# Optimization experiments

Measured on AMD Instinct MI355X. Metric: run time of the kernel, lower is better.

The kernel has to match this reference:

```python
import jax, jax.numpy as jnp
import numpy as np

L_MAX = 5
C_IN = 24
HIDDEN = 32
BATCH = 256


def _valid_pairs(l):
    return [(l1, l2) for l1 in range(L_MAX + 1) for l2 in range(L_MAX + 1)
            if abs(l1 - l2) <= l <= l1 + l2]


def _make_cg():
    # Packed padded CG coefficient tensor cg[l1, l2, l, m, m1, m2].
    # Values are fixed deterministic constants; sparsity follows the true
    # selection rule m = m1 + m2 (indices stored shifted by +l).
    D = 2 * L_MAX + 1
    rng = np.random.RandomState(42)
    cg = np.zeros((L_MAX + 1, L_MAX + 1, L_MAX + 1, D, D, D), dtype=np.float32)
    for l in range(L_MAX + 1):
        for (l1, l2) in _valid_pairs(l):
            m = np.arange(-l, l + 1)[:, None, None]
            m1 = np.arange(-l1, l1 + 1)[None, :, None]
            m2 = np.arange(-l2, l2 + 1)[None, None, :]
            mask = (m == m1 + m2).astype(np.float32)
            vals = rng.randn(2 * l + 1, 2 * l1 + 1, 2 * l2 + 1).astype(np.float32)
            cg[l1, l2, l, :2 * l + 1, :2 * l1 + 1, :2 * l2 + 1] = vals * mask
    return jnp.asarray(cg)


def setup_inputs() -> dict:
    key = jax.random.key(0)
    keys = jax.random.split(key, 12)
    inp = {}
    for l in range(L_MAX + 1):
        inp[f"x{l}"] = jax.random.normal(keys[l], (BATCH, C_IN, 2 * l + 1), dtype=jnp.float32)
    for l in range(L_MAX + 1):
        k_in = len(_valid_pairs(l)) * C_IN * C_IN
        scale = 1.0 / np.sqrt(k_in)
        inp[f"W{l}"] = jax.random.normal(keys[6 + l], (HIDDEN, k_in), dtype=jnp.float32) * scale
    inp["cg"] = _make_cg()
    return inp


def reference(x0, x1, x2, x3, x4, x5, W0, W1, W2, W3, W4, W5, cg):
    xs = [x0, x1, x2, x3, x4, x5]
    Ws = [W0, W1, W2, W3, W4, W5]
    outs = []
    for l in range(L_MAX + 1):
        feats = []
        for (l1, l2) in _valid_pairs(l):
            c = cg[l1, l2, l, :2 * l + 1, :2 * l1 + 1, :2 * l2 + 1]  # [2l+1, 2l1+1, 2l2+1]
            # P[b, c1, c2, m] = sum_{m1,m2} cg[m,m1,m2] x_l1[b,c1,m1] x_l2[b,c2,m2]
            p = jnp.einsum('mij,bci,bdj->bcdm', c, xs[l1], xs[l2])
            feats.append(p.reshape(p.shape[0], -1, 2 * l + 1))
        cat = jnp.concatenate(feats, axis=1)  # [B, n_pairs*C*C, 2l+1]
        outs.append(jnp.einsum('hk,bkm->bhm', Ws[l], cat))  # [B, HIDDEN, 2l+1]
    # concat orders along the m axis -> [B, HIDDEN, sum_l (2l+1) = 36]
    return jnp.concatenate(outs, axis=-1)
```

## Files before the change

### kernel.cpp

```cpp
#include <hip/hip_runtime.h>
#include <hip/hip_bf16.h>

typedef __attribute__((ext_vector_type(8))) short bf16x8;
typedef __attribute__((ext_vector_type(4))) float f32x4;
typedef __attribute__((ext_vector_type(2))) float f32x2;

struct Params {
  const float* x[6];
  const float* W[6];
  const float* cg;
  float* out;
  unsigned short* Wb;
};

constexpr int NPAIRS_C[6] = {6, 15, 21, 24, 24, 21};
constexpr int POFF_C[6]   = {0, 6, 21, 42, 66, 90};
constexpr size_t WBASE_C[6] = {0, 110592, 387072, 774144, 1216512, 1658880};
constexpr int KL_C[6]   = {3456, 8640, 12096, 13824, 13824, 12096};
constexpr int LOFF_C[6] = {0, 1, 4, 9, 16, 25};
#define XSTRIDE 204

constexpr int TL1[111] = {
  0,1,2,3,4,5,
  0,1,1,1,2,2,2,3,3,3,4,4,4,5,5,
  0,1,1,1,2,2,2,2,2,3,3,3,3,3,4,4,4,4,5,5,5,
  0,1,1,1,2,2,2,2,2,3,3,3,3,3,3,4,4,4,4,4,5,5,5,5,
  0,1,1,1,2,2,2,2,3,3,3,3,3,4,4,4,4,4,4,5,5,5,5,5,
  0,1,1,2,2,2,3,3,3,3,4,4,4,4,4,5,5,5,5,5,5
};
constexpr int TL2R[111] = {
  0,1,2,3,4,5,
  1,0,1,2,1,2,3,2,3,4,3,4,5,4,5,
  2,1,2,3,0,1,2,3,4,1,2,3,4,5,2,3,4,5,3,4,5,
  3,2,3,4,1,2,3,4,5,0,1,2,3,4,5,1,2,3,4,5,2,3,4,5,
  4,3,4,5,2,3,4,5,1,2,3,4,5,0,1,2,3,4,5,1,2,3,4,5,
  5,4,5,3,4,5,2,3,4,5,1,2,3,4,5,0,1,2,3,4,5
};

__constant__ int c_l1[111] = {
  0,1,2,3,4,5,
  0,1,1,1,2,2,2,3,3,3,4,4,4,5,5,
  0,1,1,1,2,2,2,2,2,3,3,3,3,3,4,4,4,4,5,5,5,
  0,1,1,1,2,2,2,2,2,3,3,3,3,3,3,4,4,4,4,4,5,5,5,5,
  0,1,1,1,2,2,2,2,3,3,3,3,3,4,4,4,4,4,4,5,5,5,5,5,
  0,1,1,2,2,2,3,3,3,3,4,4,4,4,4,5,5,5,5,5,5
};
__constant__ int c_l2[111] = {
  0,1,2,3,4,5,
  1,0,1,2,1,2,3,2,3,4,3,4,5,4,5,
  2,1,2,3,0,1,2,3,4,1,2,3,4,5,2,3,4,5,3,4,5,
  3,2,3,4,1,2,3,4,5,0,1,2,3,4,5,1,2,3,4,5,2,3,4,5,
  4,3,4,5,2,3,4,5,1,2,3,4,5,0,1,2,3,4,5,1,2,3,4,5,
  5,4,5,3,4,5,2,3,4,5,1,2,3,4,5,0,1,2,3,4,5
};
__constant__ int c_mb_l[21]  = {5,5,5,5,5,5, 4,4,4,4,4, 3,3,3,3, 2,2,2, 1,1, 0};
__constant__ int c_mb_m0[21] = {0,2,4,6,8,10, 0,2,4,6,8, 0,2,4,6, 0,2,4, 0,2, 0};
__constant__ int c_GA3[6] = {0,1,2,9,10,11};

template<int L>
__device__ __forceinline__ void swz(const Params& P, int u8) {
  constexpr int KL = KL_C[L];
  constexpr int KL8 = KL / 8;
  if (u8 >= 32 * KL8) return;
  const int h  = u8 / KL8;
  const int k  = (u8 - h * KL8) * 8;
  const int pair = k / 576;
  const int kin  = k - pair * 576;
  const int kc = kin >> 5;
  const int g  = (kin >> 3) & 3;
  const float* src = P.W[L] + (size_t)h * KL + k;
  f32x4 v0 = *(const f32x4*)src;
  f32x4 v1 = *(const f32x4*)(src + 4);
  union { __hip_bfloat162 h2; unsigned int u; } z;
  unsigned int o0, o1, o2, o3;
  z.h2 = __float22bfloat162_rn(make_float2(v0.x, v0.y)); o0 = z.u;
  z.h2 = __float22bfloat162_rn(make_float2(v0.z, v0.w)); o1 = z.u;
  z.h2 = __float22bfloat162_rn(make_float2(v1.x, v1.y)); o2 = z.u;
  z.h2 = __float22bfloat162_rn(make_float2(v1.z, v1.w)); o3 = z.u;
  const size_t dst = WBASE_C[L] + (size_t)pair * 18432 + kc * 1024 + (h >> 4) * 512
                   + ((size_t)(g * 16 + (h & 15))) * 8;
  *(uint4*)(P.Wb + dst) = make_uint4(o0, o1, o2, o3);
}

__global__ __launch_bounds__(256)
void swizzle_W(Params P) {
  const int u8 = blockIdx.x * 256 + threadIdx.x;
  switch (blockIdx.y) {
    case 0: swz<0>(P, u8); break;
    case 1: swz<1>(P, u8); break;
    case 2: swz<2>(P, u8); break;
    case 3: swz<3>(P, u8); break;
    case 4: swz<4>(P, u8); break;
    default: swz<5>(P, u8); break;
  }
}

#define XALL_F 0
#define CG_F   7344
#define RED_F  7920
#define SMEM_FLOATS 10992

template<int L>
__device__ __forceinline__ void body(const Params& P, const int mp0, const int btile) {
  constexpr int NP  = NPAIRS_C[L];
  constexpr int OFF = POFF_C[L];
  extern __shared__ float smem[];
  float* xall  = smem + XALL_F;
  float* cgall = smem + CG_F;
  float* red   = smem + RED_F;

  const int t    = threadIdx.x;
  const int lane = t & 63;
  const int w    = t >> 6;
  const int q8   = lane >> 4;
  const int rI   = lane & 15;
  const int b    = rI & 7;
  const int mpL  = rI >> 3;
  const int b0   = btile * 8;

#pragma unroll
  for (int l = 0; l < 6; ++l) {
    const int n = 2 * l + 1;
    const float* src = P.x[l] + (size_t)b0 * 24 * n;
    const int tot = 8 * 24 * n;
    for (int e = t; e < tot; e += 384) {
      const int bc = e / n;
      const int i  = e - bc * n;
      xall[(LOFF_C[l] + i) * XSTRIDE + bc] = src[e];
    }
  }
  for (int e = t; e < 2 * NP * 12; e += 384) {
    const int i  = e % 12;
    const int r  = e / 12;
    const int pi = r % NP;
    const int mL = r / NP;
    const int l1 = c_l1[OFF + pi], l2 = c_l2[OFF + pi];
    const int mp = mp0 + mL;
    const int j  = mp + l1 + l2 - L - i;
    float v = 0.f;
    if (mp <= 2 * L && i <= 2 * l1 && j >= 0 && j <= 2 * l2)
      v = P.cg[((size_t)(((l1 * 6 + l2) * 6 + L) * 11 + mp) * 11 + i) * 11 + j];
    cgall[(mL * NP + pi) * 12 + i] = v;
  }
  __syncthreads();

  f32x4 accC0 = {0.f, 0.f, 0.f, 0.f};
  f32x4 accC1 = {0.f, 0.f, 0.f, 0.f};
  const int colb = b * 24;

  const int kcA = c_GA3[w];
  const int k0  = kcA * 32 + q8 * 8;
  const int cA  = k0 / 24;
  const int d0  = k0 - cA * 24;
  const float* x2base = xall + colb + d0;
  const float* x1base = xall + colb + cA;

#pragma unroll
  for (int pi = 0; pi < NP; ++pi) {
    const int l1 = TL1[OFF + pi], l2 = TL2R[OFF + pi];
    const int n1 = 2 * l1 + 1, n2 = 2 * l2 + 1;
    const int R1 = LOFF_C[l1], R2 = LOFF_C[l2];
    const int mK0w = mp0 + l1 + l2 - L;
    const int mK0l = mK0w + mpL;
    const int i0 = (mK0w - (n2 - 1)) > 0 ? (mK0w - (n2 - 1)) : 0;
    const int i1 = (n1 - 1) < (mK0w + 1) ? (n1 - 1) : (mK0w + 1);

    const unsigned short* wbp = P.Wb + WBASE_C[L] + (size_t)pi * 18432 + lane * 8;
    const bf16x8 wfA0 = *(const bf16x8*)(wbp + kcA * 1024);
    const bf16x8 wfA1 = *(const bf16x8*)(wbp + kcA * 1024 + 512);
    const bf16x8 wfB0 = *(const bf16x8*)(wbp + (kcA + 3) * 1024);
    const bf16x8 wfB1 = *(const bf16x8*)(wbp + (kcA + 3) * 1024 + 512);
    const bf16x8 wfC0 = *(const bf16x8*)(wbp + (kcA + 6) * 1024);
    const bf16x8 wfC1 = *(const bf16x8*)(wbp + (kcA + 6) * 1024 + 512);

    f32x2 pA[4], pB[4], pC[4];
#pragma unroll
    for (int dd = 0; dd < 4; ++dd) {
      pA[dd] = (f32x2){0.f, 0.f};
      pB[dd] = (f32x2){0.f, 0.f};
      pC[dd] = (f32x2){0.f, 0.f};
    }

    const float* cgp = cgall + (mpL * NP + pi) * 12;
    for (int i = i0; i <= i1; ++i) {
      const float cgv = cgp[i];
      int j = mK0l - i;
      j = j < 0 ? 0 : (j > n2 - 1 ? n2 - 1 : j);
      const float* x2p = x2base + (R2 + j) * XSTRIDE;
      f32x2 xv[4];
      *(f32x4*)&xv[0] = *(const f32x4*)x2p;
      *(f32x4*)&xv[2] = *(const f32x4*)(x2p + 4);
      const float* x1p = x1base + (R1 + i) * XSTRIDE;
      const float sA = cgv * x1p[0];
      const float sB = cgv * x1p[4];
      const float sC = cgv * x1p[8];
      const f32x2 svA = {sA, sA}, svB = {sB, sB}, svC = {sC, sC};
#pragma unroll
      for (int dd = 0; dd < 4; ++dd) {
        pA[dd] += svA * xv[dd];
        pB[dd] += svB * xv[dd];
        pC[dd] += svC * xv[dd];
      }
    }
    union { unsigned int u[4]; bf16x8 v; } zA, zB, zC;
#pragma unroll
    for (int dd = 0; dd < 4; ++dd) {
      union { __hip_bfloat162 h2; unsigned int u; } z;
      z.h2 = __float22bfloat162_rn(make_float2(pA[dd].x, pA[dd].y)); zA.u[dd] = z.u;
      z.h2 = __float22bfloat162_rn(make_float2(pB[dd].x, pB[dd].y)); zB.u[dd] = z.u;
      z.h2 = __float22bfloat162_rn(make_float2(pC[dd].x, pC[dd].y)); zC.u[dd] = z.u;
    }
    accC0 = __builtin_amdgcn_mfma_f32_16x16x32_bf16(zA.v, wfA0, accC0, 0, 0, 0);
    accC0 = __builtin_amdgcn_mfma_f32_16x16x32_bf16(zB.v, wfB0, accC0, 0, 0, 0);
    accC0 = __builtin_amdgcn_mfma_f32_16x16x32_bf16(zC.v, wfC0, accC0, 0, 0, 0);
    accC1 = __builtin_amdgcn_mfma_f32_16x16x32_bf16(zA.v, wfA1, accC1, 0, 0, 0);
    accC1 = __builtin_amdgcn_mfma_f32_16x16x32_bf16(zB.v, wfB1, accC1, 0, 0, 0);
    accC1 = __builtin_amdgcn_mfma_f32_16x16x32_bf16(zC.v, wfC1, accC1, 0, 0, 0);
  }

  {
    const int col16 = lane & 15;
    const int rbase = w * 16 + (lane >> 4) * 4;
#pragma unroll
    for (int r = 0; r < 4; ++r) {
      red[(rbase + r) * 32 + col16]      = accC0[r];
      red[(rbase + r) * 32 + 16 + col16] = accC1[r];
    }
  }
  __syncthreads();
  for (int idx = t; idx < 512; idx += 384) {
    const int row = idx >> 5, h = idx & 31;
    float v = 0.f;
#pragma unroll
    for (int ww = 0; ww < 6; ++ww) v += red[ww * 512 + row * 32 + h];
    const int ob = row & 7, omL = row >> 3;
    const int mp = mp0 + omL;
    if (mp <= 2 * L)
      P.out[(size_t)(b0 + ob) * 1152 + h * 36 + L * L + mp] = v;
  }
}

__global__ __launch_bounds__(384, 5)
void CGLayer_main(Params P) {
  const int mb = blockIdx.x;
  const int l = c_mb_l[mb], mp0 = c_mb_m0[mb];
  const int btile = blockIdx.y;
  switch (l) {
    case 0: body<0>(P, mp0, btile); break;
    case 1: body<1>(P, mp0, btile); break;
    case 2: body<2>(P, mp0, btile); break;
    case 3: body<3>(P, mp0, btile); break;
    case 4: body<4>(P, mp0, btile); break;
    default: body<5>(P, mp0, btile); break;
  }
}

extern "C" void kernel_launch(void* const* d_in, const int* in_sizes, int n_in,
                              void* d_out, int out_size, void* d_ws, size_t ws_size,
                              hipStream_t stream) {
  Params P;
  for (int i = 0; i < 6; ++i) P.x[i] = (const float*)d_in[i];
  for (int i = 0; i < 6; ++i) P.W[i] = (const float*)d_in[6 + i];
  P.cg  = (const float*)d_in[12];
  P.out = (float*)d_out;
  P.Wb  = (unsigned short*)d_ws;

  dim3 sg(216, 6);
  swizzle_W<<<sg, 256, 0, stream>>>(P);
  dim3 grid(21, 32);
  CGLayer_main<<<grid, 384, SMEM_FLOATS * sizeof(float), stream>>>(P);
}
```

Baseline: 149.0 us.

## Specialize body on m-block offset, fully unroll CG inner loop, pad x smem layout

Turns the m-block start into a template parameter so the i-loop bounds per pair become compile-time constants, and fully unrolls the inner contraction loop. The j-index clamp is removed by adding zero guard rows and a per-lane row offset in shared memory. X storage moves to a padded per-batch stride (28) and a larger row stride, likely to cut LDS bank conflicts. This costs much more code (21 instantiations with full unrolling), which risks instruction-cache pressure, and it raises shared memory per block.

```diff
diff --git a/kernel.cpp b/kernel.cpp
--- a/kernel.cpp
+++ b/kernel.cpp
@@ -18,7 +18,8 @@
 constexpr size_t WBASE_C[6] = {0, 110592, 387072, 774144, 1216512, 1658880};
 constexpr int KL_C[6]   = {3456, 8640, 12096, 13824, 13824, 12096};
 constexpr int LOFF_C[6] = {0, 1, 4, 9, 16, 25};
-#define XSTRIDE 204
+#define XSTRIDE 236
+#define BSTRIDE 28
 
 constexpr int TL1[111] = {
   0,1,2,3,4,5,
@@ -53,8 +54,6 @@
   4,3,4,5,2,3,4,5,1,2,3,4,5,0,1,2,3,4,5,1,2,3,4,5,
   5,4,5,3,4,5,2,3,4,5,1,2,3,4,5,0,1,2,3,4,5
 };
-__constant__ int c_mb_l[21]  = {5,5,5,5,5,5, 4,4,4,4,4, 3,3,3,3, 2,2,2, 1,1, 0};
-__constant__ int c_mb_m0[21] = {0,2,4,6,8,10, 0,2,4,6,8, 0,2,4,6, 0,2,4, 0,2, 0};
 __constant__ int c_GA3[6] = {0,1,2,9,10,11};
 
 template<int L>
@@ -96,12 +95,12 @@
 }
 
 #define XALL_F 0
-#define CG_F   7344
-#define RED_F  7920
-#define SMEM_FLOATS 10992
-
-template<int L>
-__device__ __forceinline__ void body(const Params& P, const int mp0, const int btile) {
+#define CG_F   8968
+#define RED_F  9544
+#define SMEM_FLOATS 12616
+
+template<int L, int MP0>
+__device__ __forceinline__ void body(const Params& P, const int btile) {
   constexpr int NP  = NPAIRS_C[L];
   constexpr int OFF = POFF_C[L];
   extern __shared__ float smem[];
@@ -126,7 +125,9 @@
     for (int e = t; e < tot; e += 384) {
       const int bc = e / n;
       const int i  = e - bc * n;
-      xall[(LOFF_C[l] + i) * XSTRIDE + bc] = src[e];
+      const int bb = bc / 24;
+      const int cc = bc - 24 * bb;
+      xall[(1 + LOFF_C[l] + i) * XSTRIDE + bb * BSTRIDE + cc] = src[e];
     }
   }
   for (int e = t; e < 2 * NP * 12; e += 384) {
@@ -135,7 +136,7 @@
     const int pi = r % NP;
     const int mL = r / NP;
     const int l1 = c_l1[OFF + pi], l2 = c_l2[OFF + pi];
-    const int mp = mp0 + mL;
+    const int mp = MP0 + mL;
     const int j  = mp + l1 + l2 - L - i;
     float v = 0.f;
     if (mp <= 2 * L && i <= 2 * l1 && j >= 0 && j <= 2 * l2)
@@ -146,22 +147,21 @@
 
   f32x4 accC0 = {0.f, 0.f, 0.f, 0.f};
   f32x4 accC1 = {0.f, 0.f, 0.f, 0.f};
-  const int colb = b * 24;
 
   const int kcA = c_GA3[w];
   const int k0  = kcA * 32 + q8 * 8;
   const int cA  = k0 / 24;
   const int d0  = k0 - cA * 24;
-  const float* x2base = xall + colb + d0;
-  const float* x1base = xall + colb + cA;
+  const int bcol = b * BSTRIDE;
+  const float* x2l = xall + (size_t)(1 + mpL) * XSTRIDE + bcol + d0;
+  const float* x1l = xall + (size_t)1 * XSTRIDE + bcol + cA;
 
 #pragma unroll
   for (int pi = 0; pi < NP; ++pi) {
     const int l1 = TL1[OFF + pi], l2 = TL2R[OFF + pi];
     const int n1 = 2 * l1 + 1, n2 = 2 * l2 + 1;
     const int R1 = LOFF_C[l1], R2 = LOFF_C[l2];
-    const int mK0w = mp0 + l1 + l2 - L;
-    const int mK0l = mK0w + mpL;
+    const int mK0w = MP0 + l1 + l2 - L;
     const int i0 = (mK0w - (n2 - 1)) > 0 ? (mK0w - (n2 - 1)) : 0;
     const int i1 = (n1 - 1) < (mK0w + 1) ? (n1 - 1) : (mK0w + 1);
 
@@ -181,16 +181,17 @@
       pC[dd] = (f32x2){0.f, 0.f};
     }
 
-    const float* cgp = cgall + (mpL * NP + pi) * 12;
+    const float* cgp  = cgall + (mpL * NP + pi) * 12;
+    const float* x2pp = x2l + (size_t)(R2 + mK0w) * XSTRIDE;
+    const float* x1pp = x1l + (size_t)R1 * XSTRIDE;
+#pragma unroll
     for (int i = i0; i <= i1; ++i) {
       const float cgv = cgp[i];
-      int j = mK0l - i;
-      j = j < 0 ? 0 : (j > n2 - 1 ? n2 - 1 : j);
-      const float* x2p = x2base + (R2 + j) * XSTRIDE;
+      const float* x2p = x2pp - i * XSTRIDE;
       f32x2 xv[4];
       *(f32x4*)&xv[0] = *(const f32x4*)x2p;
       *(f32x4*)&xv[2] = *(const f32x4*)(x2p + 4);
-      const float* x1p = x1base + (R1 + i) * XSTRIDE;
+      const float* x1p = x1pp + i * XSTRIDE;
       const float sA = cgv * x1p[0];
       const float sB = cgv * x1p[4];
       const float sC = cgv * x1p[8];
@@ -234,7 +235,7 @@
 #pragma unroll
     for (int ww = 0; ww < 6; ++ww) v += red[ww * 512 + row * 32 + h];
     const int ob = row & 7, omL = row >> 3;
-    const int mp = mp0 + omL;
+    const int mp = MP0 + omL;
     if (mp <= 2 * L)
       P.out[(size_t)(b0 + ob) * 1152 + h * 36 + L * L + mp] = v;
   }
@@ -242,16 +243,29 @@
 
 __global__ __launch_bounds__(384, 5)
 void CGLayer_main(Params P) {
-  const int mb = blockIdx.x;
-  const int l = c_mb_l[mb], mp0 = c_mb_m0[mb];
-  const int btile = blockIdx.y;
-  switch (l) {
-    case 0: body<0>(P, mp0, btile); break;
-    case 1: body<1>(P, mp0, btile); break;
-    case 2: body<2>(P, mp0, btile); break;
-    case 3: body<3>(P, mp0, btile); break;
-    case 4: body<4>(P, mp0, btile); break;
-    default: body<5>(P, mp0, btile); break;
+  const int bt = blockIdx.y;
+  switch (blockIdx.x) {
+    case 0:  body<5, 0>(P, bt); break;
+    case 1:  body<5, 2>(P, bt); break;
+    case 2:  body<5, 4>(P, bt); break;
+    case 3:  body<5, 6>(P, bt); break;
+    case 4:  body<5, 8>(P, bt); break;
+    case 5:  body<5,10>(P, bt); break;
+    case 6:  body<4, 0>(P, bt); break;
+    case 7:  body<4, 2>(P, bt); break;
+    case 8:  body<4, 4>(P, bt); break;
+    case 9:  body<4, 6>(P, bt); break;
+    case 10: body<4, 8>(P, bt); break;
+    case 11: body<3, 0>(P, bt); break;
+    case 12: body<3, 2>(P, bt); break;
+    case 13: body<3, 4>(P, bt); break;
+    case 14: body<3, 6>(P, bt); break;
+    case 15: body<2, 0>(P, bt); break;
+    case 16: body<2, 2>(P, bt); break;
+    case 17: body<2, 4>(P, bt); break;
+    case 18: body<1, 0>(P, bt); break;
+    case 19: body<1, 2>(P, bt); break;
+    default: body<0, 0>(P, bt); break;
   }
 }
 
```

New measurement: 436.3 us. 193% more time.

## Split pair loop across two blocks with atomic output accumulation

Applied to the files above, without the earlier changes.

Doubles the grid by splitting each block's pair range into two halves, with each half accumulating into a zeroed output via atomicAdd (a memset is added before launch). The x tile in shared memory gets padding rows and a per-batch stride so the inner loop can drop the j clamp and use pointer increments. The reduction buffer now aliases the x buffer, which cuts shared-memory use and may raise occupancy. In exchange it adds an extra memset, atomics, a loop no longer fully unrolled with constant-memory lookups, and duplicated x loading per half.

```diff
diff --git a/kernel.cpp b/kernel.cpp
--- a/kernel.cpp
+++ b/kernel.cpp
@@ -17,25 +17,8 @@
 constexpr int POFF_C[6]   = {0, 6, 21, 42, 66, 90};
 constexpr size_t WBASE_C[6] = {0, 110592, 387072, 774144, 1216512, 1658880};
 constexpr int KL_C[6]   = {3456, 8640, 12096, 13824, 13824, 12096};
-constexpr int LOFF_C[6] = {0, 1, 4, 9, 16, 25};
-#define XSTRIDE 204
-
-constexpr int TL1[111] = {
-  0,1,2,3,4,5,
-  0,1,1,1,2,2,2,3,3,3,4,4,4,5,5,
-  0,1,1,1,2,2,2,2,2,3,3,3,3,3,4,4,4,4,5,5,5,
-  0,1,1,1,2,2,2,2,2,3,3,3,3,3,3,4,4,4,4,4,5,5,5,5,
-  0,1,1,1,2,2,2,2,3,3,3,3,3,4,4,4,4,4,4,5,5,5,5,5,
-  0,1,1,2,2,2,3,3,3,3,4,4,4,4,4,5,5,5,5,5,5
-};
-constexpr int TL2R[111] = {
-  0,1,2,3,4,5,
-  1,0,1,2,1,2,3,2,3,4,3,4,5,4,5,
-  2,1,2,3,0,1,2,3,4,1,2,3,4,5,2,3,4,5,3,4,5,
-  3,2,3,4,1,2,3,4,5,0,1,2,3,4,5,1,2,3,4,5,2,3,4,5,
-  4,3,4,5,2,3,4,5,1,2,3,4,5,0,1,2,3,4,5,1,2,3,4,5,
-  5,4,5,3,4,5,2,3,4,5,1,2,3,4,5,0,1,2,3,4,5
-};
+#define XSTRIDE 236
+#define BSTRIDE 28
 
 __constant__ int c_l1[111] = {
   0,1,2,3,4,5,
@@ -53,6 +36,7 @@
   4,3,4,5,2,3,4,5,1,2,3,4,5,0,1,2,3,4,5,1,2,3,4,5,
   5,4,5,3,4,5,2,3,4,5,1,2,3,4,5,0,1,2,3,4,5
 };
+__constant__ int c_loff[6] = {0, 1, 4, 9, 16, 25};
 __constant__ int c_mb_l[21]  = {5,5,5,5,5,5, 4,4,4,4,4, 3,3,3,3, 2,2,2, 1,1, 0};
 __constant__ int c_mb_m0[21] = {0,2,4,6,8,10, 0,2,4,6,8, 0,2,4,6, 0,2,4, 0,2, 0};
 __constant__ int c_GA3[6] = {0,1,2,9,10,11};
@@ -96,18 +80,18 @@
 }
 
 #define XALL_F 0
-#define CG_F   7344
-#define RED_F  7920
-#define SMEM_FLOATS 10992
+#define CG_F   8968
+#define SMEM_FLOATS 9544
 
 template<int L>
-__device__ __forceinline__ void body(const Params& P, const int mp0, const int btile) {
+__device__ __forceinline__ void body(const Params& P, const int mp0, const int btile,
+                                     const int half) {
   constexpr int NP  = NPAIRS_C[L];
   constexpr int OFF = POFF_C[L];
   extern __shared__ float smem[];
   float* xall  = smem + XALL_F;
   float* cgall = smem + CG_F;
-  float* red   = smem + RED_F;
+  float* red   = smem + XALL_F;
 
   const int t    = threadIdx.x;
   const int lane = t & 63;
@@ -117,7 +101,13 @@
   const int b    = rI & 7;
   const int mpL  = rI >> 3;
   const int b0   = btile * 8;
-
+  const int p0   = half ? NP / 2 : 0;
+  const int p1   = half ? NP : NP / 2;
+
+  for (int e = t; e < 2 * XSTRIDE; e += 384) {
+    const int r = (e < XSTRIDE) ? 0 : 37;
+    xall[r * XSTRIDE + (e % XSTRIDE)] = 0.f;
+  }
 #pragma unroll
   for (int l = 0; l < 6; ++l) {
     const int n = 2 * l + 1;
@@ -126,7 +116,9 @@
     for (int e = t; e < tot; e += 384) {
       const int bc = e / n;
       const int i  = e - bc * n;
-      xall[(LOFF_C[l] + i) * XSTRIDE + bc] = src[e];
+      const int bb = bc / 24;
+      const int cc = bc - 24 * bb;
+      xall[(1 + c_loff[l] + i) * XSTRIDE + bb * BSTRIDE + cc] = src[e];
     }
   }
   for (int e = t; e < 2 * NP * 12; e += 384) {
@@ -146,23 +138,22 @@
 
   f32x4 accC0 = {0.f, 0.f, 0.f, 0.f};
   f32x4 accC1 = {0.f, 0.f, 0.f, 0.f};
-  const int colb = b * 24;
 
   const int kcA = c_GA3[w];
   const int k0  = kcA * 32 + q8 * 8;
   const int cA  = k0 / 24;
   const int d0  = k0 - cA * 24;
-  const float* x2base = xall + colb + d0;
-  const float* x1base = xall + colb + cA;
-
-#pragma unroll
-  for (int pi = 0; pi < NP; ++pi) {
-    const int l1 = TL1[OFF + pi], l2 = TL2R[OFF + pi];
+  const int bcol = b * BSTRIDE;
+  const float* x2l = xall + (size_t)(1 + mpL) * XSTRIDE + bcol + d0;
+  const float* x1l = xall + (size_t)1 * XSTRIDE + bcol + cA;
+
+  for (int pi = p0; pi < p1; ++pi) {
+    const int l1 = c_l1[OFF + pi], l2 = c_l2[OFF + pi];
     const int n1 = 2 * l1 + 1, n2 = 2 * l2 + 1;
-    const int R1 = LOFF_C[l1], R2 = LOFF_C[l2];
+    const int R1 = c_loff[l1], R2 = c_loff[l2];
     const int mK0w = mp0 + l1 + l2 - L;
-    const int mK0l = mK0w + mpL;
-    const int i0 = (mK0w - (n2 - 1)) > 0 ? (mK0w - (n2 - 1)) : 0;
+    const int lo = mK0w - (n2 - 1);
+    const int i0 = lo > 0 ? lo : 0;
     const int i1 = (n1 - 1) < (mK0w + 1) ? (n1 - 1) : (mK0w + 1);
 
     const unsigned short* wbp = P.Wb + WBASE_C[L] + (size_t)pi * 18432 + lane * 8;
@@ -181,19 +172,18 @@
       pC[dd] = (f32x2){0.f, 0.f};
     }
 
-    const float* cgp = cgall + (mpL * NP + pi) * 12;
+    const float* cgp = cgall + (mpL * NP + pi) * 12 + i0;
+    const float* x2p = x2l + (size_t)(R2 + mK0w - i0) * XSTRIDE;
+    const float* x1p = x1l + (size_t)(R1 + i0) * XSTRIDE;
     for (int i = i0; i <= i1; ++i) {
-      const float cgv = cgp[i];
-      int j = mK0l - i;
-      j = j < 0 ? 0 : (j > n2 - 1 ? n2 - 1 : j);
-      const float* x2p = x2base + (R2 + j) * XSTRIDE;
+      const float cgv = *cgp++;
       f32x2 xv[4];
       *(f32x4*)&xv[0] = *(const f32x4*)x2p;
       *(f32x4*)&xv[2] = *(const f32x4*)(x2p + 4);
-      const float* x1p = x1base + (R1 + i) * XSTRIDE;
       const float sA = cgv * x1p[0];
       const float sB = cgv * x1p[4];
       const float sC = cgv * x1p[8];
+      x2p -= XSTRIDE; x1p += XSTRIDE;
       const f32x2 svA = {sA, sA}, svB = {sB, sB}, svC = {sC, sC};
 #pragma unroll
       for (int dd = 0; dd < 4; ++dd) {
@@ -218,6 +208,7 @@
     accC1 = __builtin_amdgcn_mfma_f32_16x16x32_bf16(zC.v, wfC1, accC1, 0, 0, 0);
   }
 
+  __syncthreads();
   {
     const int col16 = lane & 15;
     const int rbase = w * 16 + (lane >> 4) * 4;
@@ -236,7 +227,7 @@
     const int ob = row & 7, omL = row >> 3;
     const int mp = mp0 + omL;
     if (mp <= 2 * L)
-      P.out[(size_t)(b0 + ob) * 1152 + h * 36 + L * L + mp] = v;
+      atomicAdd(&P.out[(size_t)(b0 + ob) * 1152 + h * 36 + L * L + mp], v);
   }
 }
 
@@ -244,14 +235,15 @@
 void CGLayer_main(Params P) {
   const int mb = blockIdx.x;
   const int l = c_mb_l[mb], mp0 = c_mb_m0[mb];
-  const int btile = blockIdx.y;
+  const int btile = blockIdx.y >> 1;
+  const int half  = blockIdx.y & 1;
   switch (l) {
-    case 0: body<0>(P, mp0, btile); break;
-    case 1: body<1>(P, mp0, btile); break;
-    case 2: body<2>(P, mp0, btile); break;
-    case 3: body<3>(P, mp0, btile); break;
-    case 4: body<4>(P, mp0, btile); break;
-    default: body<5>(P, mp0, btile); break;
+    case 0: body<0>(P, mp0, btile, half); break;
+    case 1: body<1>(P, mp0, btile, half); break;
+    case 2: body<2>(P, mp0, btile, half); break;
+    case 3: body<3>(P, mp0, btile, half); break;
+    case 4: body<4>(P, mp0, btile, half); break;
+    default: body<5>(P, mp0, btile, half); break;
   }
 }
 
@@ -265,8 +257,9 @@
   P.out = (float*)d_out;
   P.Wb  = (unsigned short*)d_ws;
 
+  hipMemsetAsync(d_out, 0, (size_t)out_size * sizeof(float), stream);
   dim3 sg(216, 6);
   swizzle_W<<<sg, 256, 0, stream>>>(P);
-  dim3 grid(21, 32);
+  dim3 grid(21, 64);
   CGLayer_main<<<grid, 384, SMEM_FLOATS * sizeof(float), stream>>>(P);
 }
```

Result: slower. 161.7 us (+8.5%).
